# Optimization experiments

Hardware: AMD Instinct MI355X
Metric: run time of the kernel (lower is better)

## Reference

```python
import jax, jax.numpy as jnp
import numpy as np

B, I, H, DEPTH = 128, 768, 768, 8        # levels 0 (root) .. 7 (leaves)
NODES = 2 ** DEPTH - 1                    # 255 nodes, heap / level order
EPS = 1e-5                                # torch LayerNorm default


def setup_inputs() -> dict:
    key = jax.random.key(0)
    ks = jax.random.split(key, 8)
    s = 0.02  # xavier-ish scale to keep gates in a sane range
    return {
        "x": jax.random.normal(ks[0], (B, NODES, I), jnp.float32),
        "Wioux": jax.random.normal(ks[1], (DEPTH, 3 * H, I), jnp.float32) * s,
        "b_ioux": jnp.zeros((DEPTH, 3 * H), jnp.float32),
        "Wiouh": jax.random.normal(ks[2], (DEPTH, 3 * H, H), jnp.float32) * s,
        "Wfx": jax.random.normal(ks[3], (DEPTH, H, I), jnp.float32) * s,
        "b_fx": jnp.ones((DEPTH, H), jnp.float32),  # fx.bias init to ones per _init_weights
        "Wfh": jax.random.normal(ks[4], (DEPTH, H, H), jnp.float32) * s,
        "b_fh": jnp.zeros((DEPTH, H), jnp.float32),
        "ln_c_g": jnp.ones((DEPTH, H), jnp.float32),
        "ln_c_b": jnp.zeros((DEPTH, H), jnp.float32),
        "ln_h_g": jnp.ones((DEPTH, H), jnp.float32),
        "ln_h_b": jnp.zeros((DEPTH, H), jnp.float32),
        "Wout": jax.random.normal(ks[5], (H, H), jnp.float32) * s,
        "b_out": jnp.zeros((H,), jnp.float32),
    }


def _ln(v, g, b):
    m = v.mean(-1, keepdims=True)
    var = ((v - m) ** 2).mean(-1, keepdims=True)
    return (v - m) / jnp.sqrt(var + EPS) * g + b


def reference(x, Wioux, b_ioux, Wiouh, Wfx, b_fx, Wfh, b_fh,
              ln_c_g, ln_c_b, ln_h_g, ln_h_b, Wout, b_out):
    """Child-Sum TreeLSTM over a complete binary tree (heap-ordered nodes),
    processed bottom-up level-by-level; depth-l nodes use parameter set l."""
    bsz = x.shape[0]
    h = None
    for l in range(DEPTH - 1, -1, -1):       # leaves -> root
        n = 2 ** l
        xs = x[:, n - 1:2 * n - 1]            # [B, n, I] inputs at level l
        iou = jnp.einsum('bni,gi->bng', xs, Wioux[l]) + b_ioux[l]
        if h is not None:
            ch_h = h.reshape(bsz, n, 2, H)    # two children per node
            iou = iou + jnp.einsum('bnh,gh->bng', ch_h.sum(2), Wiouh[l])
        i_, o_, u_ = jnp.split(iou, 3, axis=-1)
        i_ = jax.nn.sigmoid(i_)
        o_ = jax.nn.sigmoid(o_)
        u_ = jnp.tanh(u_)
        c = i_ * u_
        if h is not None:
            fxo = jnp.einsum('bni,hi->bnh', xs, Wfx[l]) + b_fx[l]
            f = jax.nn.sigmoid(fxo[:, :, None, :]
                               + jnp.einsum('bnkh,gh->bnkg', ch_h, Wfh[l]) + b_fh[l])
            # NOTE: faithful to source: f gates multiply child *hidden* states
            c = c + (f * ch_h).sum(2)
        c = _ln(c, ln_c_g[l], ln_c_b[l])
        h = o_ * jnp.tanh(c)
        h = _ln(h, ln_h_g[l], ln_h_b[l])      # dropout is identity in eval
    h_root = h[:, 0]                          # [B, H]
    return jnp.einsum('bh,gh->bg', h_root, Wout) + b_out + x[:, 0]
```

## Files before the change

### kernel.cpp

```cpp
#include <hip/hip_runtime.h>
#include <hip/hip_bf16.h>


#define Hdim 768

typedef __hip_bfloat16 bf16;
typedef __attribute__((ext_vector_type(8))) short short8;
typedef __attribute__((ext_vector_type(4))) float floatx4;

__device__ inline float b2f(unsigned short u) {
    union { unsigned int i; float f; } v; v.i = ((unsigned int)u) << 16; return v.f;
}
__device__ inline float b2f(bf16 h) { return b2f(*(unsigned short*)&h); }
__device__ inline unsigned short f2bu(float f) {
    bf16 h = __float2bfloat16(f);
    return *(unsigned short*)&h;
}
__device__ inline ushort4 cvt4(float4 v) {
    ushort4 o; o.x = f2bu(v.x); o.y = f2bu(v.y); o.z = f2bu(v.z); o.w = f2bu(v.w);
    return o;
}
__device__ inline void ld4(const bf16* p, float* o) {
    ushort4 u = *(const ushort4*)p;
    o[0] = b2f(u.x); o[1] = b2f(u.y); o[2] = b2f(u.z); o[3] = b2f(u.w);
}
__device__ inline void st4(bf16* p, const float* v) {
    ushort4 u; u.x = f2bu(v[0]); u.y = f2bu(v[1]); u.z = f2bu(v[2]); u.w = f2bu(v[3]);
    *(ushort4*)p = u;
}

__global__ __launch_bounds__(384) void conv_wcat(
    const float* __restrict__ Wioux, const float* __restrict__ Wiouh,
    const float* __restrict__ Wfx, bf16* __restrict__ W_cat)
{
    const int row = blockIdx.x;
    const int l = row / 3072;
    const int g = row % 3072;
    const int t = threadIdx.x;
    const int k2 = t << 2;
    float4 v;
    if (g < 2304) {
        const float* src = (k2 < 768)
            ? Wioux + ((long)l * 2304 + g) * 768 + k2
            : Wiouh + ((long)l * 2304 + g) * 768 + (k2 - 768);
        v = *(const float4*)src;
    } else if (k2 < 768) {
        v = *(const float4*)(Wfx + ((long)l * 768 + (g - 2304)) * 768 + k2);
    } else {
        v = make_float4(0.f, 0.f, 0.f, 0.f);
    }
    ((ushort4*)(W_cat + (long)row * 1536))[t] = cvt4(v);
}

__global__ __launch_bounds__(256) void prep_misc(
    const float* __restrict__ Wfh, const float* __restrict__ Wout,
    const float* __restrict__ b_ioux, const float* __restrict__ b_fx,
    const float* __restrict__ x,
    bf16* __restrict__ Wfh_bf, bf16* __restrict__ Wout_bf,
    float* __restrict__ b_cat, bf16* __restrict__ leafA,
    unsigned int* __restrict__ ctrs)
{
    const int id = blockIdx.x;
    const int t = threadIdx.x;
    if (id < 4608) {
        const long i = (long)id * 256 + t;
        ((ushort4*)Wfh_bf)[i] = cvt4(((const float4*)Wfh)[i]);
    } else if (id < 5184) {
        const long i = (long)(id - 4608) * 256 + t;
        ((ushort4*)Wout_bf)[i] = cvt4(((const float4*)Wout)[i]);
    } else if (id < 5280) {
        const int i = (id - 5184) * 256 + t;
        const int l = i / 3072, g = i % 3072;
        b_cat[i] = (g < 2304) ? b_ioux[l * 2304 + g] : b_fx[l * 768 + (g - 2304)];
    } else if (id < 21664) {
        if (t < 192) {
            const int m = id - 5280;
            const int b = m >> 7, j = m & 127;
            const float* xr = x + ((long)b * 255 + 127 + j) * Hdim;
            ((ushort4*)(leafA + (long)m * Hdim))[t] = cvt4(((const float4*)xr)[t]);
        }
    } else {
        if (t < 16) ctrs[t] = 0;
    }
}

struct GemmDesc {
    const bf16* A; int lda;
    const bf16* W; int ldw;
    const float* bias;
    void* C; int ldc; int c_fp32;
    int K; int nxb;
    const float* addv; long add_stride;
};

static inline GemmDesc mkdesc(const bf16* A, int lda, const bf16* W, int ldw,
                              const float* bias, void* C, int ldc, int c_fp32,
                              int K, int nxb, const float* addv, long add_stride) {
    GemmDesc d; d.A = A; d.lda = lda; d.W = W; d.ldw = ldw; d.bias = bias;
    d.C = C; d.ldc = ldc; d.c_fp32 = c_fp32; d.K = K; d.nxb = nxb;
    d.addv = addv; d.add_stride = add_stride; return d;
}

__global__ __launch_bounds__(256) void gemm_dual(GemmDesc da, int na, GemmDesc db)
{
    __shared__ __align__(16) bf16 As[128 * 32];
    __shared__ __align__(16) bf16 Ws[128 * 32];
    int id = blockIdx.x;
    const bool second = (id >= na);
    if (second) id -= na;
    const GemmDesc d = second ? db : da;
    const int bm = id / d.nxb, bn = id % d.nxb;

    const int t = threadIdx.x;
    const int wave = t >> 6, lane = t & 63;
    const long m_blk = (long)bm << 7;
    const long n_blk = (long)bn << 7;

    const int srow = (wave << 5) + (lane >> 2);
    const int sbyte = (lane & 3) << 4;
    const char* gA = (const char*)(d.A + (m_blk + srow) * (long)d.lda) + sbyte;
    const char* gW = (const char*)(d.W + (n_blk + srow) * (long)d.ldw) + sbyte;
    const long aRow16 = (long)d.lda * 32;
    const long wRow16 = (long)d.ldw * 32;
    bf16* lA = As + (wave << 10);
    bf16* lW = Ws + (wave << 10);

    floatx4 zero = {0.f, 0.f, 0.f, 0.f};
    floatx4 acc[4][4];
#pragma unroll
    for (int i = 0; i < 4; i++)
#pragma unroll
        for (int j = 0; j < 4; j++) acc[i][j] = zero;

    const int mrow = (wave & 1) << 6;
    const int ncol = (wave >> 1) << 6;
    const short* AsS = (const short*)As;
    const short* WsS = (const short*)Ws;
    const int fm = lane & 15;
    const int fk = (lane >> 4) << 3;

    for (int k0 = 0; k0 < d.K; k0 += 32) {
        __builtin_amdgcn_global_load_lds(
            (const __attribute__((address_space(1))) unsigned int*)gA,
            (__attribute__((address_space(3))) unsigned int*)lA, 16, 0, 0);
        __builtin_amdgcn_global_load_lds(
            (const __attribute__((address_space(1))) unsigned int*)(gA + aRow16),
            (__attribute__((address_space(3))) unsigned int*)(lA + 512), 16, 0, 0);
        __builtin_amdgcn_global_load_lds(
            (const __attribute__((address_space(1))) unsigned int*)gW,
            (__attribute__((address_space(3))) unsigned int*)lW, 16, 0, 0);
        __builtin_amdgcn_global_load_lds(
            (const __attribute__((address_space(1))) unsigned int*)(gW + wRow16),
            (__attribute__((address_space(3))) unsigned int*)(lW + 512), 16, 0, 0);
        gA += 64; gW += 64;
        __syncthreads();

        short8 af[4], bfr[4];
#pragma unroll
        for (int i = 0; i < 4; i++) {
            af[i]  = *(const short8*)(AsS + (mrow + i * 16 + fm) * 32 + fk);
            bfr[i] = *(const short8*)(WsS + (ncol + i * 16 + fm) * 32 + fk);
        }
#pragma unroll
        for (int i = 0; i < 4; i++)
#pragma unroll
            for (int j = 0; j < 4; j++)
                acc[i][j] = __builtin_amdgcn_mfma_f32_16x16x32_bf16(
                    af[i], bfr[j], acc[i][j], 0, 0, 0);
        __syncthreads();
    }

    const int crow0 = (lane >> 4) << 2;
    const int ccol = lane & 15;
#pragma unroll
    for (int i = 0; i < 4; i++) {
#pragma unroll
        for (int j = 0; j < 4; j++) {
            const long col = n_blk + ncol + j * 16 + ccol;
            const float bv = d.bias ? d.bias[col] : 0.f;
#pragma unroll
            for (int r = 0; r < 4; r++) {
                const long row = m_blk + mrow + i * 16 + crow0 + r;
                float v = acc[i][j][r] + bv;
                if (d.addv) v += d.addv[row * d.add_stride + col];
                if (d.c_fp32) ((float*)d.C)[row * (long)d.ldc + col] = v;
                else ((bf16*)d.C)[row * (long)d.ldc + col] = __float2bfloat16(v);
            }
        }
    }
}

__global__ __launch_bounds__(512, 2) void gemm8_dual(
    GemmDesc da, int na, GemmDesc db, int ntot, unsigned int* __restrict__ ctr)
{
    __shared__ __align__(16) char smem[131072];
    __shared__ int sjob;

    const int tid = threadIdx.x;
    const int w = tid >> 6, lane = tid & 63;

    const int colb = (((lane & 7) ^ ((lane >> 3) & 7)) << 4);
    const int rw = (w << 4) + (lane >> 3);
    const int fm = lane & 15;
    const int fkB = (lane >> 4) << 4;
    const int sx = (lane & 7) << 4;
    const int cx0 = fkB ^ sx;
    const int cx1 = cx0 ^ 64;
    const int arow0 = ((w >> 2) << 7) + fm;
    const int brow0 = ((w & 3) << 6) + fm;
    char* lW = smem + (w << 11);

    for (;;) {
        __syncthreads();
        if (tid == 0) sjob = (int)atomicAdd(ctr, 1u);
        __syncthreads();
        int id = sjob;
        if (id >= ntot) return;
        const bool second = (id >= na);
        if (second) id -= na;
        const GemmDesc d = second ? db : da;
        const int bm = id / d.nxb, bn = id % d.nxb;
        const long m_blk = (long)bm << 8;
        const long n_blk = (long)bn << 8;
        const int T = d.K >> 6;

        const long ldaB = (long)d.lda * 2, ldwB = (long)d.ldw * 2;
        const char* gA0 = (const char*)(d.A + m_blk * d.lda) + (long)rw * ldaB + colb;
        const char* gB0 = (const char*)(d.W + n_blk * d.ldw) + (long)rw * ldwB + colb;
        const long aH = ldaB << 7, bH = ldwB << 7;
        const long a8 = ldaB << 3, b8 = ldwB << 3;

        auto stageA = [&](int tile, int buf, int half) {
            const char* g = gA0 + (half ? aH : 0) + ((long)tile << 7);
            char* l = lW + buf * 32768 + half * 16384;
            __builtin_amdgcn_global_load_lds(
                (const __attribute__((address_space(1))) unsigned int*)g,
                (__attribute__((address_space(3))) unsigned int*)l, 16, 0, 0);
            __builtin_amdgcn_global_load_lds(
                (const __attribute__((address_space(1))) unsigned int*)(g + a8),
                (__attribute__((address_space(3))) unsigned int*)(l + 1024), 16, 0, 0);
        };
        auto stageB = [&](int tile, int buf, int half) {
            const char* g = gB0 + (half ? bH : 0) + ((long)tile << 7);
            char* l = lW + 65536 + buf * 32768 + half * 16384;
            __builtin_amdgcn_global_load_lds(
                (const __attribute__((address_space(1))) unsigned int*)g,
                (__attribute__((address_space(3))) unsigned int*)l, 16, 0, 0);
            __builtin_amdgcn_global_load_lds(
                (const __attribute__((address_space(1))) unsigned int*)(g + b8),
                (__attribute__((address_space(3))) unsigned int*)(l + 1024), 16, 0, 0);
        };

        floatx4 acc[8][4];
        const floatx4 fzero = {0.f, 0.f, 0.f, 0.f};
#pragma unroll
        for (int i = 0; i < 8; i++)
#pragma unroll
            for (int j = 0; j < 4; j++) acc[i][j] = fzero;

        stageA(0, 0, 0); stageA(0, 0, 1); stageB(0, 0, 0); stageB(0, 0, 1);
        if (T > 1) {
            stageB(1, 1, 0); stageB(1, 1, 1); stageA(1, 1, 0);
            asm volatile("s_waitcnt vmcnt(6)" ::: "memory");
        } else {
            asm volatile("s_waitcnt vmcnt(0)" ::: "memory");
        }
        __builtin_amdgcn_sched_barrier(0);
        __builtin_amdgcn_s_barrier();
        __builtin_amdgcn_sched_barrier(0);

        short8 a[4][2], b[4][2];
        for (int tt = 0; tt < T; ++tt) {
            const int buf = tt & 1;
            const char* la = smem + buf * 32768;
            const char* lb = smem + 65536 + buf * 32768;
#pragma unroll
            for (int mf = 0; mf < 4; ++mf) {
                a[mf][0] = *(const short8*)(la + ((arow0 + mf * 16) << 7) + cx0);
                a[mf][1] = *(const short8*)(la + ((arow0 + mf * 16) << 7) + cx1);
            }
#pragma unroll
            for (int nf = 0; nf < 2; ++nf) {
                b[nf][0] = *(const short8*)(lb + ((brow0 + nf * 16) << 7) + cx0);
                b[nf][1] = *(const short8*)(lb + ((brow0 + nf * 16) << 7) + cx1);
            }
            if (tt + 1 < T) stageA(tt + 1, buf ^ 1, 1);
            __builtin_amdgcn_s_barrier();
            asm volatile("s_waitcnt lgkmcnt(0)" ::: "memory");
            __builtin_amdgcn_sched_barrier(0);
            __builtin_amdgcn_s_setprio(1);
#pragma unroll
            for (int ks = 0; ks < 2; ++ks)
#pragma unroll
                for (int mf = 0; mf < 4; ++mf)
#pragma unroll
                    for (int nf = 0; nf < 2; ++nf)
                        acc[mf][nf] = __builtin_amdgcn_mfma_f32_16x16x32_bf16(
                            a[mf][ks], b[nf][ks], acc[mf][nf], 0, 0, 0);
            __builtin_amdgcn_s_setprio(0);
            __builtin_amdgcn_s_barrier();
            __builtin_amdgcn_sched_barrier(0);
#pragma unroll
            for (int nf = 0; nf < 2; ++nf) {
                b[2 + nf][0] = *(const short8*)(lb + ((brow0 + (2 + nf) * 16) << 7) + cx0);
                b[2 + nf][1] = *(const short8*)(lb + ((brow0 + (2 + nf) * 16) << 7) + cx1);
            }
            __builtin_amdgcn_s_barrier();
            asm volatile("s_waitcnt lgkmcnt(0)" ::: "memory");
            __builtin_amdgcn_sched_barrier(0);
            __builtin_amdgcn_s_setprio(1);
#pragma unroll
            for (int ks = 0; ks < 2; ++ks)
#pragma unroll
                for (int mf = 0; mf < 4; ++mf)
#pragma unroll
                    for (int nf = 0; nf < 2; ++nf)
                        acc[mf][2 + nf] = __builtin_amdgcn_mfma_f32_16x16x32_bf16(
                            a[mf][ks], b[2 + nf][ks], acc[mf][2 + nf], 0, 0, 0);
            __builtin_amdgcn_s_setprio(0);
            __builtin_amdgcn_s_barrier();
            __builtin_amdgcn_sched_barrier(0);
#pragma unroll
            for (int mf = 0; mf < 4; ++mf) {
                a[mf][0] = *(const short8*)(la + ((arow0 + (4 + mf) * 16) << 7) + cx0);
                a[mf][1] = *(const short8*)(la + ((arow0 + (4 + mf) * 16) << 7) + cx1);
            }
            if (tt + 2 < T) stageB(tt + 2, buf, 0);
            __builtin_amdgcn_s_barrier();
            asm volatile("s_waitcnt lgkmcnt(0)" ::: "memory");
            __builtin_amdgcn_sched_barrier(0);
            __builtin_amdgcn_s_setprio(1);
#pragma unroll
            for (int ks = 0; ks < 2; ++ks)
#pragma unroll
                for (int mf = 0; mf < 4; ++mf)
#pragma unroll
                    for (int nf = 0; nf < 2; ++nf)
                        acc[4 + mf][2 + nf] = __builtin_amdgcn_mfma_f32_16x16x32_bf16(
                            a[mf][ks], b[2 + nf][ks], acc[4 + mf][2 + nf], 0, 0, 0);
            __builtin_amdgcn_s_setprio(0);
            __builtin_amdgcn_s_barrier();
            __builtin_amdgcn_sched_barrier(0);
            if (tt + 2 < T) { stageB(tt + 2, buf, 1); stageA(tt + 2, buf, 0); }
            __builtin_amdgcn_s_setprio(1);
#pragma unroll
            for (int ks = 0; ks < 2; ++ks)
#pragma unroll
                for (int mf = 0; mf < 4; ++mf)
#pragma unroll
                    for (int nf = 0; nf < 2; ++nf)
                        acc[4 + mf][nf] = __builtin_amdgcn_mfma_f32_16x16x32_bf16(
                            a[mf][ks], b[nf][ks], acc[4 + mf][nf], 0, 0, 0);
            __builtin_amdgcn_s_setprio(0);
            if (tt + 1 < T) {
                if (tt + 2 < T) asm volatile("s_waitcnt vmcnt(6)" ::: "memory");
                else            asm volatile("s_waitcnt vmcnt(0)" ::: "memory");
                __builtin_amdgcn_sched_barrier(0);
                __builtin_amdgcn_s_barrier();
                __builtin_amdgcn_sched_barrier(0);
            }
        }

        const int crow = (lane >> 4) << 2;
        const int ccol = lane & 15;
        const long row0 = m_blk + ((long)(w >> 2) << 7);
        const long col0 = n_blk + ((w & 3) << 6);
#pragma unroll
        for (int mf = 0; mf < 8; ++mf) {
#pragma unroll
            for (int nf = 0; nf < 4; ++nf) {
                const long col = col0 + nf * 16 + ccol;
                const float bv = d.bias ? d.bias[col] : 0.f;
#pragma unroll
                for (int r = 0; r < 4; ++r) {
                    const long row = row0 + mf * 16 + crow + r;
                    const float v = acc[mf][nf][r] + bv;
                    if (d.c_fp32) ((float*)d.C)[row * (long)d.ldc + col] = v;
                    else ((bf16*)d.C)[row * (long)d.ldc + col] = __float2bfloat16(v);
                }
            }
        }
    }
}

__device__ inline float sigf(float x) { return 1.f / (1.f + __expf(-x)); }
__device__ inline float tanh_fast(float x) { return 2.f / (1.f + __expf(-2.f * x)) - 1.f; }

__device__ inline void block_reduce4(float& a, float& b, float& c, float& d,
                                     float* s) {
#pragma unroll
    for (int off = 32; off > 0; off >>= 1) {
        a += __shfl_down(a, off, 64);
        b += __shfl_down(b, off, 64);
        c += __shfl_down(c, off, 64);
        d += __shfl_down(d, off, 64);
    }
    const int lane = threadIdx.x & 63, w = threadIdx.x >> 6;
    __syncthreads();
    if (lane == 0) { s[w] = a; s[w + 4] = b; s[w + 8] = c; s[w + 12] = d; }
    __syncthreads();
    a = s[0] + s[1] + s[2] + s[3];
    b = s[4] + s[5] + s[6] + s[7];
    c = s[8] + s[9] + s[10] + s[11];
    d = s[12] + s[13] + s[14] + s[15];
}

__global__ __launch_bounds__(256) void pointwise_pair(
    const bf16* __restrict__ C, int ldc,
    const bf16* __restrict__ fhb,
    const bf16* __restrict__ hprev2,
    const float* __restrict__ x,
    const float* __restrict__ bfh,
    const float* __restrict__ gc, const float* __restrict__ bc,
    const float* __restrict__ gh, const float* __restrict__ bh,
    bf16* __restrict__ hout,
    bf16* __restrict__ Anext,
    int m0, int lp)
{
    __shared__ float sred[16];
    const int pl = blockIdx.x;
    const int t = threadIdx.x;
    const bool act = t < 192;
    const int j = t << 2;
    const bf16* cr0 = C + (long)(2 * pl) * ldc;
    const bf16* cr1 = cr0 + ldc;
    float c0v[4], c1v[4], o0v[4], o1v[4], h0v[4], h1v[4];
    float s0 = 0.f, q0 = 0.f, s1 = 0.f, q1 = 0.f;
    if (act) {
        float i0[4], i1[4], u0[4], u1[4];
        ld4(cr0 + j, i0); ld4(cr1 + j, i1);
        ld4(cr0 + Hdim + j, o0v); ld4(cr1 + Hdim + j, o1v);
        ld4(cr0 + 2 * Hdim + j, u0); ld4(cr1 + 2 * Hdim + j, u1);
        if (fhb) {
            float fx0[4], fx1[4], fb0[4], fb1[4], fb2[4], fb3[4];
            float hp0[4], hp1[4], hp2[4], hp3[4];
            ld4(cr0 + 3 * Hdim + j, fx0); ld4(cr1 + 3 * Hdim + j, fx1);
            const long base = (long)(4 * pl) * Hdim + j;
            ld4(fhb + base, fb0); ld4(fhb + base + Hdim, fb1);
            ld4(fhb + base + 2 * Hdim, fb2); ld4(fhb + base + 3 * Hdim, fb3);
            ld4(hprev2 + base, hp0); ld4(hprev2 + base + Hdim, hp1);
            ld4(hprev2 + base + 2 * Hdim, hp2); ld4(hprev2 + base + 3 * Hdim, hp3);
            const float4 bf4 = *(const float4*)(bfh + j);
#pragma unroll
            for (int q = 0; q < 4; q++) {
                const float bq = (&bf4.x)[q];
                float c0 = sigf(i0[q]) * tanh_fast(u0[q]);
                float c1 = sigf(i1[q]) * tanh_fast(u1[q]);
                c0 += sigf(fx0[q] + fb0[q] + bq) * hp0[q]
                    + sigf(fx0[q] + fb1[q] + bq) * hp1[q];
                c1 += sigf(fx1[q] + fb2[q] + bq) * hp2[q]
                    + sigf(fx1[q] + fb3[q] + bq) * hp3[q];
                c0v[q] = c0; c1v[q] = c1;
                s0 += c0; q0 += c0 * c0; s1 += c1; q1 += c1 * c1;
            }
        } else {
#pragma unroll
            for (int q = 0; q < 4; q++) {
                const float c0 = sigf(i0[q]) * tanh_fast(u0[q]);
                const float c1 = sigf(i1[q]) * tanh_fast(u1[q]);
                c0v[q] = c0; c1v[q] = c1;
                s0 += c0; q0 += c0 * c0; s1 += c1; q1 += c1 * c1;
            }
        }
    }
    block_reduce4(s0, q0, s1, q1, sred);
    const float m0c = s0 / Hdim, m1c = s1 / Hdim;
    const float r0c = rsqrtf(q0 / Hdim - m0c * m0c + 1e-5f);
    const float r1c = rsqrtf(q1 / Hdim - m1c * m1c + 1e-5f);
    float hs0 = 0.f, hq0 = 0.f, hs1 = 0.f, hq1 = 0.f;
    if (act) {
        const float4 gc4 = *(const float4*)(gc + j);
        const float4 bc4 = *(const float4*)(bc + j);
#pragma unroll
        for (int q = 0; q < 4; q++) {
            const float cn0 = (c0v[q] - m0c) * r0c * (&gc4.x)[q] + (&bc4.x)[q];
            const float cn1 = (c1v[q] - m1c) * r1c * (&gc4.x)[q] + (&bc4.x)[q];
            const float h0 = sigf(o0v[q]) * tanh_fast(cn0);
            const float h1 = sigf(o1v[q]) * tanh_fast(cn1);
            h0v[q] = h0; h1v[q] = h1;
            hs0 += h0; hq0 += h0 * h0; hs1 += h1; hq1 += h1 * h1;
        }
    }
    block_reduce4(hs0, hq0, hs1, hq1, sred);
    const float mh0 = hs0 / Hdim, mh1 = hs1 / Hdim;
    const float rh0 = rsqrtf(hq0 / Hdim - mh0 * mh0 + 1e-5f);
    const float rh1 = rsqrtf(hq1 / Hdim - mh1 * mh1 + 1e-5f);

    if (act) {
        const int pg = m0 / 2 + pl;
        const int b = pg >> lp;
        const int jn = pg & ((1 << lp) - 1);
        const float* xr = x + ((long)b * 255 + (1 << lp) - 1 + jn) * Hdim;
        bf16* arow = Anext + (long)pg * 1536;
        const float4 gh4 = *(const float4*)(gh + j);
        const float4 bh4 = *(const float4*)(bh + j);
        const float4 xr4 = *(const float4*)(xr + j);
        float hh0[4], hh1[4], ha[4], xs[4];
#pragma unroll
        for (int q = 0; q < 4; q++) {
            hh0[q] = (h0v[q] - mh0) * rh0 * (&gh4.x)[q] + (&bh4.x)[q];
            hh1[q] = (h1v[q] - mh1) * rh1 * (&gh4.x)[q] + (&bh4.x)[q];
            ha[q] = hh0[q] + hh1[q];
            xs[q] = (&xr4.x)[q];
        }
        st4(hout + (long)(2 * pl) * Hdim + j, hh0);
        st4(hout + (long)(2 * pl + 1) * Hdim + j, hh1);
        st4(arow + 768 + j, ha);
        st4(arow + j, xs);
    }
}

__global__ __launch_bounds__(256) void pointwise_root(
    const bf16* __restrict__ C, int ldc,
    const bf16* __restrict__ fhb, const bf16* __restrict__ hprev,
    const float* __restrict__ bfh,
    const float* __restrict__ gc, const float* __restrict__ bc,
    const float* __restrict__ gh, const float* __restrict__ bh,
    bf16* __restrict__ hout)
{
    __shared__ float sred[16];
    const int m = blockIdx.x;
    const int t = threadIdx.x;
    const bool act = t < 192;
    const int j = t << 2;
    const bf16* cr = C + (long)m * ldc;
    float cv[4], ov[4], hv[4];
    float ssum = 0.f, ssq = 0.f, d0 = 0.f, d1 = 0.f;
    if (act) {
        float iv[4], uv[4], fx[4], fb0[4], fb1[4], hp0[4], hp1[4];
        ld4(cr + j, iv); ld4(cr + Hdim + j, ov); ld4(cr + 2 * Hdim + j, uv);
        ld4(cr + 3 * Hdim + j, fx);
        const long base = (long)(2 * m) * Hdim + j;
        ld4(fhb + base, fb0); ld4(fhb + base + Hdim, fb1);
        ld4(hprev + base, hp0); ld4(hprev + base + Hdim, hp1);
        const float4 bf4 = *(const float4*)(bfh + j);
#pragma unroll
        for (int q = 0; q < 4; q++) {
            const float bq = (&bf4.x)[q];
            float c = sigf(iv[q]) * tanh_fast(uv[q]);
            c += sigf(fx[q] + fb0[q] + bq) * hp0[q]
               + sigf(fx[q] + fb1[q] + bq) * hp1[q];
            cv[q] = c; ssum += c; ssq += c * c;
        }
    }
    block_reduce4(ssum, ssq, d0, d1, sred);
    const float mean = ssum / Hdim;
    const float rstd = rsqrtf(ssq / Hdim - mean * mean + 1e-5f);
    float hs = 0.f, hq = 0.f;
    if (act) {
        const float4 gc4 = *(const float4*)(gc + j);
        const float4 bc4 = *(const float4*)(bc + j);
#pragma unroll
        for (int q = 0; q < 4; q++) {
            const float cn = (cv[q] - mean) * rstd * (&gc4.x)[q] + (&bc4.x)[q];
            const float h = sigf(ov[q]) * tanh_fast(cn);
            hv[q] = h; hs += h; hq += h * h;
        }
    }
    d0 = 0.f; d1 = 0.f;
    block_reduce4(hs, hq, d0, d1, sred);
    const float mh = hs / Hdim;
    const float rh = rsqrtf(hq / Hdim - mh * mh + 1e-5f);
    if (act) {
        const float4 gh4 = *(const float4*)(gh + j);
        const float4 bh4 = *(const float4*)(bh + j);
        float hh[4];
#pragma unroll
        for (int q = 0; q < 4; q++)
            hh[q] = (hv[q] - mh) * rh * (&gh4.x)[q] + (&bh4.x)[q];
        st4(hout + (long)m * Hdim + j, hh);
    }
}

extern "C" void kernel_launch(void* const* d_in, const int* in_sizes, int n_in,
                              void* d_out, int out_size, void* d_ws, size_t ws_size,
                              hipStream_t stream) {
    (void)in_sizes; (void)n_in; (void)out_size; (void)ws_size;
    const float* x      = (const float*)d_in[0];
    const float* Wioux  = (const float*)d_in[1];
    const float* b_ioux = (const float*)d_in[2];
    const float* Wiouh  = (const float*)d_in[3];
    const float* Wfx    = (const float*)d_in[4];
    const float* b_fx   = (const float*)d_in[5];
    const float* Wfh    = (const float*)d_in[6];
    const float* b_fh   = (const float*)d_in[7];
    const float* ln_c_g = (const float*)d_in[8];
    const float* ln_c_b = (const float*)d_in[9];
    const float* ln_h_g = (const float*)d_in[10];
    const float* ln_h_b = (const float*)d_in[11];
    const float* Wout   = (const float*)d_in[12];
    const float* b_out  = (const float*)d_in[13];
    float* out = (float*)d_out;

    char* p = (char*)d_ws;
    bf16* W_cat   = (bf16*)p; p += 8L * 3072 * 1536 * 2;
    bf16* Wfh_bf  = (bf16*)p; p += 8L * 768 * 768 * 2;
    bf16* Wout_bf = (bf16*)p; p += 768L * 768 * 2;
    float* b_cat  = (float*)p; p += 8L * 3072 * 4;
    bf16* leafA   = (bf16*)p; p += 16384L * 768 * 2;
    bf16* A6      = (bf16*)p; p += 8192L * 1536 * 2;
    bf16* A5      = (bf16*)p; p += 4096L * 1536 * 2;
    bf16* Cbuf    = (bf16*)p; p += 4096L * 3072 * 2;
    bf16* hA      = (bf16*)p; p += 16384L * 768 * 2;
    bf16* hB      = (bf16*)p; p += 8192L * 768 * 2;
    unsigned int* ctrs = (unsigned int*)p; p += 64;
    bf16* fhb     = leafA;
    bf16* Cleaf   = A5;

    conv_wcat<<<8 * 3072, 384, 0, stream>>>(Wioux, Wiouh, Wfx, W_cat);
    prep_misc<<<5280 + 16384 + 1, 256, 0, stream>>>(
        Wfh, Wout, b_ioux, b_fx, x, Wfh_bf, Wout_bf, b_cat, leafA, ctrs);

    GemmDesc dummy = mkdesc(nullptr, 0, nullptr, 0, nullptr, nullptr, 0, 0, 0, 1,
                            nullptr, 0);
    int kc = 0;

    {
        const int cm0[3] = {0, 5632, 11264};
        const int cmc[3] = {5632, 5632, 5120};
        for (int c = 0; c < 3; c++) {
            const int m0 = cm0[c], Mc = cmc[c];
            GemmDesc dl = mkdesc(leafA + (long)m0 * 768, 768,
                                 W_cat + 7L * 3072 * 1536, 1536, b_cat + 7 * 3072,
                                 Cleaf, 2304, 0, 768, 9, nullptr, 0);
            const int ntot = (Mc / 256) * 9;
            gemm8_dual<<<(ntot < 256 ? ntot : 256), 512, 0, stream>>>(
                dl, ntot, dummy, ntot, ctrs + kc++);
            pointwise_pair<<<Mc / 2, 256, 0, stream>>>(
                Cleaf, 2304, nullptr, nullptr, x, nullptr,
                ln_c_g + 7 * Hdim, ln_c_b + 7 * Hdim, ln_h_g + 7 * Hdim, ln_h_b + 7 * Hdim,
                hA + (long)m0 * Hdim, A6, m0, 6);
        }
    }

    const int CH = 4096;
    bf16* hp = hA; bf16* hc = hB;
    bf16* Acur = A6; bf16* Anxt = A5;
    for (int l = 6; l >= 1; l--) {
        const int M = 128 << l;
        const int Mc = (M < CH) ? M : CH;
        const int nch = M / Mc;
        for (int c = 0; c < nch; c++) {
            const int m0 = c * Mc;
            if (l >= 5) {
                GemmDesc diou = mkdesc(Acur + (long)m0 * 1536, 1536,
                                       W_cat + (long)l * 3072 * 1536, 1536,
                                       b_cat + l * 3072, Cbuf, 3072, 0, 1536, 12,
                                       nullptr, 0);
                GemmDesc dfh = mkdesc(hp + (long)2 * m0 * Hdim, 768,
                                      Wfh_bf + (long)l * 768 * 768, 768, nullptr,
                                      fhb, 768, 0, 768, 3, nullptr, 0);
                const int na = 12 * (Mc / 256);
                const int nb = 3 * (2 * Mc / 256);
                const int ntot = na + nb;
                gemm8_dual<<<(ntot < 256 ? ntot : 256), 512, 0, stream>>>(
                    diou, na, dfh, ntot, ctrs + kc++);
            } else {
                GemmDesc diou = mkdesc(Acur + (long)m0 * 1536, 1536,
                                       W_cat + (long)l * 3072 * 1536, 1536,
                                       b_cat + l * 3072, Cbuf, 3072, 0, 1536, 24,
                                       nullptr, 0);
                GemmDesc dfh = mkdesc(hp + (long)2 * m0 * Hdim, 768,
                                      Wfh_bf + (long)l * 768 * 768, 768, nullptr,
                                      fhb, 768, 0, 768, 6, nullptr, 0);
                const int na = 24 * (Mc / 128);
                const int nb = 6 * (2 * Mc / 128);
                gemm_dual<<<na + nb, 256, 0, stream>>>(diou, na, dfh);
            }
            pointwise_pair<<<Mc / 2, 256, 0, stream>>>(
                Cbuf, 3072, fhb, hp + (long)2 * m0 * Hdim, x, b_fh + l * Hdim,
                ln_c_g + l * Hdim, ln_c_b + l * Hdim, ln_h_g + l * Hdim, ln_h_b + l * Hdim,
                hc + (long)m0 * Hdim, Anxt, m0, l - 1);
        }
        bf16* t1 = hp; hp = hc; hc = t1;
        bf16* t2 = Acur; Acur = Anxt; Anxt = t2;
    }

    {
        GemmDesc diou = mkdesc(Acur, 1536, W_cat, 1536, b_cat, Cbuf, 3072, 0,
                               1536, 24, nullptr, 0);
        GemmDesc dfh = mkdesc(hp, 768, Wfh_bf, 768, nullptr, fhb, 768, 0,
                              768, 6, nullptr, 0);
        gemm_dual<<<24 + 12, 256, 0, stream>>>(diou, 24, dfh);
        pointwise_root<<<128, 256, 0, stream>>>(
            Cbuf, 3072, fhb, hp, b_fh,
            ln_c_g, ln_c_b, ln_h_g, ln_h_b, hc);
    }

    {
        GemmDesc dout = mkdesc(hc, 768, Wout_bf, 768, b_out, out, 768, 1,
                               768, 6, x, 255L * 768);
        gemm_dual<<<6, 256, 0, stream>>>(dout, 6, dummy);
    }
}
```

Before: 990.0 us.

## Add split-K to small-level GEMMs and reduce partials in pointwise kernels

Small upper-tree GEMMs (levels 4..0 and the output projection) are split along K into 2-4 slices so more blocks are launched. The partial products are written as separate slices and summed in the pointwise kernels, or in a new out_reduce kernel for the output. This targets low GPU occupancy at small M, at the cost of extra partial-sum memory traffic, bf16 rounding of partials, and one extra launch.

```diff
diff --git a/kernel.cpp b/kernel.cpp
--- a/kernel.cpp
+++ b/kernel.cpp
@@ -89,16 +89,21 @@
     const bf16* W; int ldw;
     const float* bias;
     void* C; int ldc; int c_fp32;
-    int K; int nxb;
+    int K;
+    int nxb;
     const float* addv; long add_stride;
+    int nps;
+    long cslice;
 };
 
 static inline GemmDesc mkdesc(const bf16* A, int lda, const bf16* W, int ldw,
                               const float* bias, void* C, int ldc, int c_fp32,
-                              int K, int nxb, const float* addv, long add_stride) {
+                              int K, int nxb, const float* addv, long add_stride,
+                              int nps, long cslice) {
     GemmDesc d; d.A = A; d.lda = lda; d.W = W; d.ldw = ldw; d.bias = bias;
     d.C = C; d.ldc = ldc; d.c_fp32 = c_fp32; d.K = K; d.nxb = nxb;
-    d.addv = addv; d.add_stride = add_stride; return d;
+    d.addv = addv; d.add_stride = add_stride; d.nps = nps; d.cslice = cslice;
+    return d;
 }
 
 __global__ __launch_bounds__(256) void gemm_dual(GemmDesc da, int na, GemmDesc db)
@@ -109,7 +114,12 @@
     const bool second = (id >= na);
     if (second) id -= na;
     const GemmDesc d = second ? db : da;
+    const int s = id / d.nps; id -= s * d.nps;
     const int bm = id / d.nxb, bn = id % d.nxb;
+    const bf16* Ag = d.A + (long)s * d.K;
+    const bf16* Wg = d.W + (long)s * d.K;
+    char* Cg = (char*)d.C + (long)s * d.cslice;
+    const float* bias = (s == 0) ? d.bias : nullptr;
 
     const int t = threadIdx.x;
     const int wave = t >> 6, lane = t & 63;
@@ -118,8 +128,8 @@
 
     const int srow = (wave << 5) + (lane >> 2);
     const int sbyte = (lane & 3) << 4;
-    const char* gA = (const char*)(d.A + (m_blk + srow) * (long)d.lda) + sbyte;
-    const char* gW = (const char*)(d.W + (n_blk + srow) * (long)d.ldw) + sbyte;
+    const char* gA = (const char*)(Ag + (m_blk + srow) * (long)d.lda) + sbyte;
+    const char* gW = (const char*)(Wg + (n_blk + srow) * (long)d.ldw) + sbyte;
     const long aRow16 = (long)d.lda * 32;
     const long wRow16 = (long)d.ldw * 32;
     bf16* lA = As + (wave << 10);
@@ -177,14 +187,14 @@
 #pragma unroll
         for (int j = 0; j < 4; j++) {
             const long col = n_blk + ncol + j * 16 + ccol;
-            const float bv = d.bias ? d.bias[col] : 0.f;
+            const float bv = bias ? bias[col] : 0.f;
 #pragma unroll
             for (int r = 0; r < 4; r++) {
                 const long row = m_blk + mrow + i * 16 + crow0 + r;
                 float v = acc[i][j][r] + bv;
                 if (d.addv) v += d.addv[row * d.add_stride + col];
-                if (d.c_fp32) ((float*)d.C)[row * (long)d.ldc + col] = v;
-                else ((bf16*)d.C)[row * (long)d.ldc + col] = __float2bfloat16(v);
+                if (d.c_fp32) ((float*)Cg)[row * (long)d.ldc + col] = v;
+                else ((bf16*)Cg)[row * (long)d.ldc + col] = __float2bfloat16(v);
             }
         }
     }
@@ -406,8 +416,8 @@
 }
 
 __global__ __launch_bounds__(256) void pointwise_pair(
-    const bf16* __restrict__ C, int ldc,
-    const bf16* __restrict__ fhb,
+    const bf16* __restrict__ C, int ldc, int ns, long csl,
+    const bf16* __restrict__ fhb, int nsf, long fsl,
     const bf16* __restrict__ hprev2,
     const float* __restrict__ x,
     const float* __restrict__ bfh,
@@ -424,20 +434,64 @@
     const int j = t << 2;
     const bf16* cr0 = C + (long)(2 * pl) * ldc;
     const bf16* cr1 = cr0 + ldc;
-    float c0v[4], c1v[4], o0v[4], o1v[4], h0v[4], h1v[4];
+    float c0v[4], c1v[4], h0v[4], h1v[4];
+    float o0v[4] = {0, 0, 0, 0}, o1v[4] = {0, 0, 0, 0};
     float s0 = 0.f, q0 = 0.f, s1 = 0.f, q1 = 0.f;
     if (act) {
-        float i0[4], i1[4], u0[4], u1[4];
-        ld4(cr0 + j, i0); ld4(cr1 + j, i1);
-        ld4(cr0 + Hdim + j, o0v); ld4(cr1 + Hdim + j, o1v);
-        ld4(cr0 + 2 * Hdim + j, u0); ld4(cr1 + 2 * Hdim + j, u1);
+        float i0[4] = {0, 0, 0, 0}, i1[4] = {0, 0, 0, 0};
+        float u0[4] = {0, 0, 0, 0}, u1[4] = {0, 0, 0, 0};
+        float fx0[4] = {0, 0, 0, 0}, fx1[4] = {0, 0, 0, 0};
+        float tv[4];
+        for (int s = 0; s < ns; ++s) {
+            const bf16* c0s = cr0 + (long)s * csl;
+            const bf16* c1s = cr1 + (long)s * csl;
+            ld4(c0s + j, tv);
+#pragma unroll
+            for (int q = 0; q < 4; q++) i0[q] += tv[q];
+            ld4(c1s + j, tv);
+#pragma unroll
+            for (int q = 0; q < 4; q++) i1[q] += tv[q];
+            ld4(c0s + Hdim + j, tv);
+#pragma unroll
+            for (int q = 0; q < 4; q++) o0v[q] += tv[q];
+            ld4(c1s + Hdim + j, tv);
+#pragma unroll
+            for (int q = 0; q < 4; q++) o1v[q] += tv[q];
+            ld4(c0s + 2 * Hdim + j, tv);
+#pragma unroll
+            for (int q = 0; q < 4; q++) u0[q] += tv[q];
+            ld4(c1s + 2 * Hdim + j, tv);
+#pragma unroll
+            for (int q = 0; q < 4; q++) u1[q] += tv[q];
+            if (fhb) {
+                ld4(c0s + 3 * Hdim + j, tv);
+#pragma unroll
+                for (int q = 0; q < 4; q++) fx0[q] += tv[q];
+                ld4(c1s + 3 * Hdim + j, tv);
+#pragma unroll
+                for (int q = 0; q < 4; q++) fx1[q] += tv[q];
+            }
+        }
         if (fhb) {
-            float fx0[4], fx1[4], fb0[4], fb1[4], fb2[4], fb3[4];
+            float fb0[4] = {0, 0, 0, 0}, fb1[4] = {0, 0, 0, 0};
+            float fb2[4] = {0, 0, 0, 0}, fb3[4] = {0, 0, 0, 0};
+            const long base = (long)(4 * pl) * Hdim + j;
+            for (int s = 0; s < nsf; ++s) {
+                const bf16* fs = fhb + (long)s * fsl + base;
+                ld4(fs, tv);
+#pragma unroll
+                for (int q = 0; q < 4; q++) fb0[q] += tv[q];
+                ld4(fs + Hdim, tv);
+#pragma unroll
+                for (int q = 0; q < 4; q++) fb1[q] += tv[q];
+                ld4(fs + 2 * Hdim, tv);
+#pragma unroll
+                for (int q = 0; q < 4; q++) fb2[q] += tv[q];
+                ld4(fs + 3 * Hdim, tv);
+#pragma unroll
+                for (int q = 0; q < 4; q++) fb3[q] += tv[q];
+            }
             float hp0[4], hp1[4], hp2[4], hp3[4];
-            ld4(cr0 + 3 * Hdim + j, fx0); ld4(cr1 + 3 * Hdim + j, fx1);
-            const long base = (long)(4 * pl) * Hdim + j;
-            ld4(fhb + base, fb0); ld4(fhb + base + Hdim, fb1);
-            ld4(fhb + base + 2 * Hdim, fb2); ld4(fhb + base + 3 * Hdim, fb3);
             ld4(hprev2 + base, hp0); ld4(hprev2 + base + Hdim, hp1);
             ld4(hprev2 + base + 2 * Hdim, hp2); ld4(hprev2 + base + 3 * Hdim, hp3);
             const float4 bf4 = *(const float4*)(bfh + j);
@@ -511,8 +565,9 @@
 }
 
 __global__ __launch_bounds__(256) void pointwise_root(
-    const bf16* __restrict__ C, int ldc,
-    const bf16* __restrict__ fhb, const bf16* __restrict__ hprev,
+    const bf16* __restrict__ C, int ldc, int ns, long csl,
+    const bf16* __restrict__ fhb, int nsf, long fsl,
+    const bf16* __restrict__ hprev,
     const float* __restrict__ bfh,
     const float* __restrict__ gc, const float* __restrict__ bc,
     const float* __restrict__ gh, const float* __restrict__ bh,
@@ -524,14 +579,39 @@
     const bool act = t < 192;
     const int j = t << 2;
     const bf16* cr = C + (long)m * ldc;
-    float cv[4], ov[4], hv[4];
+    float cv[4], hv[4];
+    float ov[4] = {0, 0, 0, 0};
     float ssum = 0.f, ssq = 0.f, d0 = 0.f, d1 = 0.f;
     if (act) {
-        float iv[4], uv[4], fx[4], fb0[4], fb1[4], hp0[4], hp1[4];
-        ld4(cr + j, iv); ld4(cr + Hdim + j, ov); ld4(cr + 2 * Hdim + j, uv);
-        ld4(cr + 3 * Hdim + j, fx);
+        float iv[4] = {0, 0, 0, 0}, uv[4] = {0, 0, 0, 0}, fx[4] = {0, 0, 0, 0};
+        float tv[4];
+        for (int s = 0; s < ns; ++s) {
+            const bf16* cs = cr + (long)s * csl;
+            ld4(cs + j, tv);
+#pragma unroll
+            for (int q = 0; q < 4; q++) iv[q] += tv[q];
+            ld4(cs + Hdim + j, tv);
+#pragma unroll
+            for (int q = 0; q < 4; q++) ov[q] += tv[q];
+            ld4(cs + 2 * Hdim + j, tv);
+#pragma unroll
+            for (int q = 0; q < 4; q++) uv[q] += tv[q];
+            ld4(cs + 3 * Hdim + j, tv);
+#pragma unroll
+            for (int q = 0; q < 4; q++) fx[q] += tv[q];
+        }
+        float fb0[4] = {0, 0, 0, 0}, fb1[4] = {0, 0, 0, 0};
         const long base = (long)(2 * m) * Hdim + j;
-        ld4(fhb + base, fb0); ld4(fhb + base + Hdim, fb1);
+        for (int s = 0; s < nsf; ++s) {
+            const bf16* fs = fhb + (long)s * fsl + base;
+            ld4(fs, tv);
+#pragma unroll
+            for (int q = 0; q < 4; q++) fb0[q] += tv[q];
+            ld4(fs + Hdim, tv);
+#pragma unroll
+            for (int q = 0; q < 4; q++) fb1[q] += tv[q];
+        }
+        float hp0[4], hp1[4];
         ld4(hprev + base, hp0); ld4(hprev + base + Hdim, hp1);
         const float4 bf4 = *(const float4*)(bfh + j);
 #pragma unroll
@@ -570,6 +650,23 @@
             hh[q] = (hv[q] - mh) * rh * (&gh4.x)[q] + (&bh4.x)[q];
         st4(hout + (long)m * Hdim + j, hh);
     }
+}
+
+__global__ __launch_bounds__(192) void out_reduce(
+    const float* __restrict__ P, long psl, int ns,
+    const float* __restrict__ b_out, const float* __restrict__ x,
+    float* __restrict__ out)
+{
+    const int m = blockIdx.x;
+    const int j = threadIdx.x << 2;
+    float4 a = *(const float4*)(b_out + j);
+    const float4 xv = *(const float4*)(x + (long)m * 255 * 768 + j);
+    a.x += xv.x; a.y += xv.y; a.z += xv.z; a.w += xv.w;
+    for (int s = 0; s < ns; ++s) {
+        const float4 pv = *(const float4*)(P + (long)s * psl + (long)m * 768 + j);
+        a.x += pv.x; a.y += pv.y; a.z += pv.z; a.w += pv.w;
+    }
+    *(float4*)(out + (long)m * 768 + j) = a;
 }
 
 extern "C" void kernel_launch(void* const* d_in, const int* in_sizes, int n_in,
@@ -604,6 +701,7 @@
     bf16* hA      = (bf16*)p; p += 16384L * 768 * 2;
     bf16* hB      = (bf16*)p; p += 8192L * 768 * 2;
     unsigned int* ctrs = (unsigned int*)p; p += 64;
+    float* outP   = (float*)p; p += 128L * 768 * 4 * 4;
     bf16* fhb     = leafA;
     bf16* Cleaf   = A5;
 
@@ -612,7 +710,7 @@
         Wfh, Wout, b_ioux, b_fx, x, Wfh_bf, Wout_bf, b_cat, leafA, ctrs);
 
     GemmDesc dummy = mkdesc(nullptr, 0, nullptr, 0, nullptr, nullptr, 0, 0, 0, 1,
-                            nullptr, 0);
+                            nullptr, 0, 1, 0);
     int kc = 0;
 
     {
@@ -622,53 +720,43 @@
             const int m0 = cm0[c], Mc = cmc[c];
             GemmDesc dl = mkdesc(leafA + (long)m0 * 768, 768,
                                  W_cat + 7L * 3072 * 1536, 1536, b_cat + 7 * 3072,
-                                 Cleaf, 2304, 0, 768, 9, nullptr, 0);
+                                 Cleaf, 2304, 0, 768, 9, nullptr, 0,
+                                 (Mc / 256) * 9, 0);
             const int ntot = (Mc / 256) * 9;
             gemm8_dual<<<(ntot < 256 ? ntot : 256), 512, 0, stream>>>(
                 dl, ntot, dummy, ntot, ctrs + kc++);
             pointwise_pair<<<Mc / 2, 256, 0, stream>>>(
-                Cleaf, 2304, nullptr, nullptr, x, nullptr,
+                Cleaf, 2304, 1, 0, nullptr, 1, 0, nullptr, x, nullptr,
                 ln_c_g + 7 * Hdim, ln_c_b + 7 * Hdim, ln_h_g + 7 * Hdim, ln_h_b + 7 * Hdim,
                 hA + (long)m0 * Hdim, A6, m0, 6);
         }
     }
 
-    const int CH = 4096;
     bf16* hp = hA; bf16* hc = hB;
     bf16* Acur = A6; bf16* Anxt = A5;
-    for (int l = 6; l >= 1; l--) {
+
+    for (int l = 6; l >= 5; l--) {
         const int M = 128 << l;
-        const int Mc = (M < CH) ? M : CH;
+        const int Mc = 4096;
         const int nch = M / Mc;
         for (int c = 0; c < nch; c++) {
             const int m0 = c * Mc;
-            if (l >= 5) {
-                GemmDesc diou = mkdesc(Acur + (long)m0 * 1536, 1536,
-                                       W_cat + (long)l * 3072 * 1536, 1536,
-                                       b_cat + l * 3072, Cbuf, 3072, 0, 1536, 12,
-                                       nullptr, 0);
-                GemmDesc dfh = mkdesc(hp + (long)2 * m0 * Hdim, 768,
-                                      Wfh_bf + (long)l * 768 * 768, 768, nullptr,
-                                      fhb, 768, 0, 768, 3, nullptr, 0);
-                const int na = 12 * (Mc / 256);
-                const int nb = 3 * (2 * Mc / 256);
-                const int ntot = na + nb;
-                gemm8_dual<<<(ntot < 256 ? ntot : 256), 512, 0, stream>>>(
-                    diou, na, dfh, ntot, ctrs + kc++);
-            } else {
-                GemmDesc diou = mkdesc(Acur + (long)m0 * 1536, 1536,
-                                       W_cat + (long)l * 3072 * 1536, 1536,
-                                       b_cat + l * 3072, Cbuf, 3072, 0, 1536, 24,
-                                       nullptr, 0);
-                GemmDesc dfh = mkdesc(hp + (long)2 * m0 * Hdim, 768,
-                                      Wfh_bf + (long)l * 768 * 768, 768, nullptr,
-                                      fhb, 768, 0, 768, 6, nullptr, 0);
-                const int na = 24 * (Mc / 128);
-                const int nb = 6 * (2 * Mc / 128);
-                gemm_dual<<<na + nb, 256, 0, stream>>>(diou, na, dfh);
-            }
+            GemmDesc diou = mkdesc(Acur + (long)m0 * 1536, 1536,
+                                   W_cat + (long)l * 3072 * 1536, 1536,
+                                   b_cat + l * 3072, Cbuf, 3072, 0, 1536, 12,
+                                   nullptr, 0, 12 * (Mc / 256), 0);
+            GemmDesc dfh = mkdesc(hp + (long)2 * m0 * Hdim, 768,
+                                  Wfh_bf + (long)l * 768 * 768, 768, nullptr,
+                                  fhb, 768, 0, 768, 3, nullptr, 0,
+                                  3 * (2 * Mc / 256), 0);
+            const int na = 12 * (Mc / 256);
+            const int nb = 3 * (2 * Mc / 256);
+            const int ntot = na + nb;
+            gemm8_dual<<<(ntot < 256 ? ntot : 256), 512, 0, stream>>>(
+                diou, na, dfh, ntot, ctrs + kc++);
             pointwise_pair<<<Mc / 2, 256, 0, stream>>>(
-                Cbuf, 3072, fhb, hp + (long)2 * m0 * Hdim, x, b_fh + l * Hdim,
+                Cbuf, 3072, 1, 0, fhb, 1, 0, hp + (long)2 * m0 * Hdim,
+                x, b_fh + l * Hdim,
                 ln_c_g + l * Hdim, ln_c_b + l * Hdim, ln_h_g + l * Hdim, ln_h_b + l * Hdim,
                 hc + (long)m0 * Hdim, Anxt, m0, l - 1);
         }
@@ -676,20 +764,50 @@
         bf16* t2 = Acur; Acur = Anxt; Anxt = t2;
     }
 
+    for (int l = 4; l >= 1; l--) {
+        const int M = 128 << l;
+        const int Si = (l == 4) ? 2 : 4;
+        const int Sf = (l == 4) ? 2 : 4;
+        const int Ki = 1536 / Si;
+        const int Kf = 768 / Sf;
+        const int npsA = (M / 128) * 24;
+        const int npsB = (2 * M / 128) * 6;
+        GemmDesc diou = mkdesc(Acur, 1536,
+                               W_cat + (long)l * 3072 * 1536, 1536,
+                               b_cat + l * 3072, Cbuf, 3072, 0, Ki, 24,
+                               nullptr, 0, npsA, (long)M * 3072 * 2);
+        GemmDesc dfh = mkdesc(hp, 768,
+                              Wfh_bf + (long)l * 768 * 768, 768, nullptr,
+                              fhb, 768, 0, Kf, 6,
+                              nullptr, 0, npsB, (long)2 * M * 768 * 2);
+        const int na = Si * npsA;
+        const int nb = Sf * npsB;
+        gemm_dual<<<na + nb, 256, 0, stream>>>(diou, na, dfh);
+        pointwise_pair<<<M / 2, 256, 0, stream>>>(
+            Cbuf, 3072, Si, (long)M * 3072, fhb, Sf, (long)2 * M * 768,
+            hp, x, b_fh + l * Hdim,
+            ln_c_g + l * Hdim, ln_c_b + l * Hdim, ln_h_g + l * Hdim, ln_h_b + l * Hdim,
+            hc, Anxt, 0, l - 1);
+        bf16* t1 = hp; hp = hc; hc = t1;
+        bf16* t2 = Acur; Acur = Anxt; Anxt = t2;
+    }
+
     {
         GemmDesc diou = mkdesc(Acur, 1536, W_cat, 1536, b_cat, Cbuf, 3072, 0,
-                               1536, 24, nullptr, 0);
+                               384, 24, nullptr, 0, 24, 128L * 3072 * 2);
         GemmDesc dfh = mkdesc(hp, 768, Wfh_bf, 768, nullptr, fhb, 768, 0,
-                              768, 6, nullptr, 0);
-        gemm_dual<<<24 + 12, 256, 0, stream>>>(diou, 24, dfh);
+                              384, 6, nullptr, 0, 12, 256L * 768 * 2);
+        const int na = 4 * 24, nb = 2 * 12;
+        gemm_dual<<<na + nb, 256, 0, stream>>>(diou, na, dfh);
         pointwise_root<<<128, 256, 0, stream>>>(
-            Cbuf, 3072, fhb, hp, b_fh,
+            Cbuf, 3072, 4, 128L * 3072, fhb, 2, 256L * 768, hp, b_fh,
             ln_c_g, ln_c_b, ln_h_g, ln_h_b, hc);
     }
 
     {
-        GemmDesc dout = mkdesc(hc, 768, Wout_bf, 768, b_out, out, 768, 1,
-                               768, 6, x, 255L * 768);
-        gemm_dual<<<6, 256, 0, stream>>>(dout, 6, dummy);
-    }
-}
+        GemmDesc dout = mkdesc(hc, 768, Wout_bf, 768, nullptr, outP, 768, 1,
+                               192, 6, nullptr, 0, 6, 128L * 768 * 4);
+        gemm_dual<<<4 * 6, 256, 0, stream>>>(dout, 4 * 6, dummy);
+        out_reduce<<<128, 192, 0, stream>>>(outP, 128L * 768, 4, b_out, x, out);
+    }
+}
```

New measurement: 895.0 us. 9.6% less time.
